# Kernel tuning notes

Measured on AMD Instinct MI355X. Metric: run time of the kernel, lower is better.

## Reference

```python
import jax, jax.numpy as jnp
import numpy as np

N_NODES = 100000
N_EDGES = 1600000
N_GRAPHS = 128
ATOM_F = 92
BOND_F = 41
EMB = 64
HID = 128
CHG = 16
N_LAYERS = 3
EPS = 1e-5


def setup_inputs() -> dict:
    key = jax.random.key(0)
    ks = jax.random.split(key, 32)
    s = 0.05
    inp = {
        "x": jax.random.normal(ks[0], (N_NODES, ATOM_F), jnp.float32),
        "edge_attr": jax.random.uniform(ks[1], (N_EDGES, BOND_F), jnp.float32),
        "charge": jax.random.normal(ks[2], (N_GRAPHS,), jnp.float32),
        "edge_index": jax.random.randint(ks[3], (2, N_EDGES), 0, N_NODES),
        "batch": jnp.sort(jax.random.randint(ks[4], (N_NODES,), 0, N_GRAPHS)),
        # embeddings
        "W_charge": jax.random.normal(ks[5], (1, CHG), jnp.float32) * s,
        "b_charge": jnp.zeros((CHG,), jnp.float32),
        "W_atom": jax.random.normal(ks[6], (ATOM_F + CHG, EMB), jnp.float32) * s,
        "b_atom": jnp.zeros((EMB,), jnp.float32),
        "W_bond": jax.random.normal(ks[7], (BOND_F, EMB), jnp.float32) * s,
        "b_bond": jnp.zeros((EMB,), jnp.float32),
        # conv layers (stacked over layer dim)
        "conv_eW1": jax.random.normal(ks[8], (N_LAYERS, 3 * EMB, EMB), jnp.float32) * s,
        "conv_eb1": jnp.zeros((N_LAYERS, EMB), jnp.float32),
        "conv_eW2": jax.random.normal(ks[9], (N_LAYERS, EMB, EMB), jnp.float32) * s,
        "conv_eb2": jnp.zeros((N_LAYERS, EMB), jnp.float32),
        "conv_nW1": jax.random.normal(ks[10], (N_LAYERS, 2 * EMB, EMB), jnp.float32) * s,
        "conv_nb1": jnp.zeros((N_LAYERS, EMB), jnp.float32),
        "conv_nW2": jax.random.normal(ks[11], (N_LAYERS, EMB, EMB), jnp.float32) * s,
        "conv_nb2": jnp.zeros((N_LAYERS, EMB), jnp.float32),
        "bn_gamma": jnp.ones((N_LAYERS, EMB), jnp.float32),
        "bn_beta": jnp.zeros((N_LAYERS, EMB), jnp.float32),
        # predictor
        "pW1": jax.random.normal(ks[12], (EMB, HID), jnp.float32) * s,
        "pb1": jnp.zeros((HID,), jnp.float32),
        "pW2": jax.random.normal(ks[13], (HID, HID), jnp.float32) * s,
        "pb2": jnp.zeros((HID,), jnp.float32),
        "pW3": jax.random.normal(ks[14], (HID, 1), jnp.float32) * s,
        "pb3": jnp.zeros((1,), jnp.float32),
    }
    return inp


def reference(x, edge_attr, charge, W_charge, b_charge, W_atom, b_atom,
              W_bond, b_bond, conv_eW1, conv_eb1, conv_eW2, conv_eb2,
              conv_nW1, conv_nb1, conv_nW2, conv_nb2, bn_gamma, bn_beta,
              pW1, pb1, pW2, pb2, pW3, pb3, edge_index, batch):
    sp = jax.nn.softplus
    n_nodes = x.shape[0]
    n_graphs = charge.shape[0]

    # early charge integration: per-graph charge embedding broadcast to nodes
    charge_feat = charge[:, None] @ W_charge + b_charge          # [B, CHG]
    x = jnp.concatenate([x, charge_feat[batch]], axis=1)          # [N, ATOM_F+CHG]
    x = x @ W_atom + b_atom                                       # [N, EMB]
    ea = edge_attr @ W_bond + b_bond                              # [E, EMB]

    row, col = edge_index[0], edge_index[1]
    for i in range(conv_eW1.shape[0]):
        xr, xc = x[row], x[col]                                   # gathers [E, EMB]
        # edge update: MLP on [x_row, x_col, edge_attr]
        e_in = jnp.concatenate([xr, xc, ea], axis=1)              # [E, 3*EMB]
        ea = sp(e_in @ conv_eW1[i] + conv_eb1[i]) @ conv_eW2[i] + conv_eb2[i]
        # node messages: MLP on [x_row, new edge_attr]
        m_in = jnp.concatenate([xr, ea], axis=1)                  # [E, 2*EMB]
        msg = sp(m_in @ conv_nW1[i] + conv_nb1[i]) @ conv_nW2[i] + conv_nb2[i]
        x_new = jax.ops.segment_sum(msg, col, num_segments=n_nodes)
        # BatchNorm1d (training-mode batch stats, biased variance)
        mean = jnp.mean(x_new, axis=0)
        var = jnp.var(x_new, axis=0)
        x_new = (x_new - mean) * jax.lax.rsqrt(var + EPS) * bn_gamma[i] + bn_beta[i]
        x = sp(x_new) + x                                         # residual

    # global mean pool over graphs
    sums = jax.ops.segment_sum(x, batch, num_segments=n_graphs)   # [B, EMB]
    cnt = jax.ops.segment_sum(jnp.ones((n_nodes, 1), x.dtype), batch, num_segments=n_graphs)
    g = sums / jnp.maximum(cnt, 1.0)

    # predictor MLP (dropout is identity in eval mode)
    h = sp(g @ pW1 + pb1)
    h = sp(h @ pW2 + pb2)
    out = h @ pW3 + pb3                                           # [B, 1]
    return out.squeeze(-1)
```

## Files before the change

### kernel.cpp

```cpp
#include <hip/hip_runtime.h>
#include <math.h>

typedef short v8s __attribute__((ext_vector_type(8)));
typedef float v4f __attribute__((ext_vector_type(4)));

__device__ __forceinline__ float sp_f(float x) {
  return fmaxf(x, 0.0f) + 0.69314718056f * __log2f(1.0f + __expf(-fabsf(x)));
}

__device__ __forceinline__ unsigned short f2bf(float f) {
  union { float f; unsigned u; } x; x.f = f;
  unsigned r = (x.u + 0x7FFF + ((x.u >> 16) & 1)) >> 16;
  return (unsigned short)r;
}

__device__ __forceinline__ float bf2f(unsigned short h) {
  union { unsigned u; float f; } x; x.u = ((unsigned)h) << 16;
  return x.f;
}

__global__ __launch_bounds__(256) void k_prep_wfrag(
    const float* __restrict__ eW1, const float* __restrict__ eW2,
    const float* __restrict__ nW1, const float* __restrict__ nW2,
    unsigned short* __restrict__ wfrag) {
  int i = blockIdx.x >> 2;
  int m = blockIdx.x & 3;
  const float* W;
  if (m == 0)      W = eW1 + (size_t)i * 192 * 64 + 128 * 64;
  else if (m == 1) W = eW2 + (size_t)i * 64 * 64;
  else if (m == 2) W = nW1 + (size_t)i * 128 * 64 + 64 * 64;
  else             W = nW2 + (size_t)i * 64 * 64;
  unsigned short* out = wfrag + ((size_t)i * 4 + m) * 4096;
  for (int f = threadIdx.x; f < 4096; f += 256) {
    int j = f & 7, ln = (f >> 3) & 63, kh = (f >> 9) & 1, ct = f >> 10;
    int k = kh * 32 + (ln >> 4) * 8 + j;
    int n = ct * 16 + (ln & 15);
    out[f] = f2bf(W[k * 64 + n]);
  }
}

__global__ __launch_bounds__(256) void k_embed_nodes(
    const float* __restrict__ x, const int* __restrict__ batch,
    const float* __restrict__ charge, const float* __restrict__ W_charge,
    const float* __restrict__ b_charge, const float* __restrict__ W_atom,
    const float* __restrict__ b_atom, float* __restrict__ xemb, int N) {
  __shared__ float sW[108 * 64];
  __shared__ float sX[128 * 92];
  __shared__ float sb[64];
  __shared__ float sWc[16];
  __shared__ float sbc[16];
  for (int i = threadIdx.x; i < 108 * 64; i += blockDim.x) sW[i] = W_atom[i];
  if (threadIdx.x < 64) sb[threadIdx.x] = b_atom[threadIdx.x];
  if (threadIdx.x < 16) {
    sWc[threadIdx.x] = W_charge[threadIdx.x];
    sbc[threadIdx.x] = b_charge[threadIdx.x];
  }
  int ntiles = (N + 127) >> 7;
  for (int tile = blockIdx.x; tile < ntiles; tile += gridDim.x) {
    int base = tile << 7;
    int cnt = N - base; if (cnt > 128) cnt = 128;
    __syncthreads();
    if (cnt == 128) {
      const float4* src = (const float4*)(x + (size_t)base * 92);
      for (int i = threadIdx.x; i < 2944; i += 256) ((float4*)sX)[i] = src[i];
    } else {
      for (int i = threadIdx.x; i < cnt * 92; i += 256)
        sX[i] = x[(size_t)base * 92 + i];
    }
    __syncthreads();
    int t = threadIdx.x;
    int node = t & 127, half = t >> 7;
    if (node < cnt) {
      int n = base + node;
      float acc[32];
#pragma unroll
      for (int j = 0; j < 32; ++j) acc[j] = sb[half * 32 + j];
      const float* xr = sX + node * 92;
      for (int k = 0; k < 92; ++k) {
        float a = xr[k];
        const float* wk = sW + k * 64 + half * 32;
#pragma unroll
        for (int j = 0; j < 32; ++j) acc[j] = fmaf(a, wk[j], acc[j]);
      }
      float ch = charge[batch[n]];
#pragma unroll
      for (int c = 0; c < 16; ++c) {
        float cf = fmaf(ch, sWc[c], sbc[c]);
        const float* wk = sW + (92 + c) * 64 + half * 32;
#pragma unroll
        for (int j = 0; j < 32; ++j) acc[j] = fmaf(cf, wk[j], acc[j]);
      }
      float* o = xemb + (size_t)n * 64 + half * 32;
#pragma unroll
      for (int q8 = 0; q8 < 8; ++q8)
        ((float4*)o)[q8] = make_float4(acc[4*q8], acc[4*q8+1], acc[4*q8+2], acc[4*q8+3]);
    }
  }
}

__global__ __launch_bounds__(256) void k_hist(const int* __restrict__ col,
                                              int* __restrict__ counts, int E) {
  int stride = gridDim.x * blockDim.x;
  for (int e = blockIdx.x * blockDim.x + threadIdx.x; e < E; e += stride)
    atomicAdd(&counts[col[e]], 1);
}

__global__ __launch_bounds__(256) void k_scan1(const int* __restrict__ counts,
                                               int* __restrict__ scan_tmp,
                                               int* __restrict__ bsum, int N) {
  __shared__ int sd[2][256];
  int t = threadIdx.x;
  int i = blockIdx.x * 256 + t;
  int v = (i < N) ? counts[i] : 0;
  sd[0][t] = v;
  __syncthreads();
  int s = 0;
#pragma unroll
  for (int off = 1; off < 256; off <<= 1) {
    int nv = sd[s][t];
    if (t >= off) nv += sd[s][t - off];
    sd[s ^ 1][t] = nv;
    s ^= 1;
    __syncthreads();
  }
  if (i < N) scan_tmp[i] = sd[s][t];
  if (t == 255) bsum[blockIdx.x] = sd[s][255];
}

__global__ __launch_bounds__(256) void k_scan2(int* __restrict__ b, int NB) {
  __shared__ int sd[2][256];
  __shared__ int carry_s;
  int t = threadIdx.x;
  if (t == 0) carry_s = 0;
  __syncthreads();
  for (int base = 0; base < NB; base += 256) {
    int i = base + t;
    int v = (i < NB) ? b[i] : 0;
    sd[0][t] = v;
    __syncthreads();
    int s = 0;
#pragma unroll
    for (int off = 1; off < 256; off <<= 1) {
      int nv = sd[s][t];
      if (t >= off) nv += sd[s][t - off];
      sd[s ^ 1][t] = nv;
      s ^= 1;
      __syncthreads();
    }
    int c = carry_s;
    int tot = sd[s][255];
    if (i < NB) b[i] = sd[s][t] + c;
    __syncthreads();
    if (t == 0) carry_s = c + tot;
    __syncthreads();
  }
}

__global__ __launch_bounds__(256) void k_scan3(const int* __restrict__ counts,
                                               const int* __restrict__ scan_tmp,
                                               const int* __restrict__ bsum,
                                               int* __restrict__ cursor, int N) {
  int i = blockIdx.x * 256 + threadIdx.x;
  if (i < N) {
    int base = (blockIdx.x > 0) ? bsum[blockIdx.x - 1] : 0;
    cursor[i] = scan_tmp[i] - counts[i] + base;
  }
}

__global__ __launch_bounds__(256) void k_scatter(
    const int* __restrict__ row, const int* __restrict__ col,
    int* __restrict__ cursor, int* __restrict__ pos,
    int* __restrict__ row_s, int* __restrict__ col_s, int E) {
  int stride = gridDim.x * blockDim.x;
  for (int e = blockIdx.x * blockDim.x + threadIdx.x; e < E; e += stride) {
    int c = col[e];
    int p = atomicAdd(&cursor[c], 1);
    pos[e] = p;
    row_s[p] = row[e];
    col_s[p] = c;
  }
}

__global__ __launch_bounds__(256) void k_embed_bonds_pos(
    const float* __restrict__ eattr, const int* __restrict__ pos,
    const float* __restrict__ W_bond, const float* __restrict__ b_bond,
    unsigned short* __restrict__ ea16, int E) {
  __shared__ float sW[41 * 64];
  __shared__ float sE[256 * 41];
  __shared__ float sb[64];
  for (int i = threadIdx.x; i < 41 * 64; i += blockDim.x) sW[i] = W_bond[i];
  if (threadIdx.x < 64) sb[threadIdx.x] = b_bond[threadIdx.x];
  int ntiles = (E + 255) >> 8;
  for (int tile = blockIdx.x; tile < ntiles; tile += gridDim.x) {
    int base = tile << 8;
    int cnt = E - base; if (cnt > 256) cnt = 256;
    __syncthreads();
    if (cnt == 256) {
      const float4* src = (const float4*)(eattr + (size_t)base * 41);
      for (int i = threadIdx.x; i < 2624; i += 256) ((float4*)sE)[i] = src[i];
    } else {
      for (int i = threadIdx.x; i < cnt * 41; i += 256)
        sE[i] = eattr[(size_t)base * 41 + i];
    }
    __syncthreads();
    int t = threadIdx.x;
    if (t < cnt) {
      float acc[64];
#pragma unroll
      for (int j = 0; j < 64; ++j) acc[j] = sb[j];
      const float* er = sE + t * 41;
      for (int k = 0; k < 41; ++k) {
        float a = er[k];
        const float* wk = sW + k * 64;
#pragma unroll
        for (int j = 0; j < 64; ++j) acc[j] = fmaf(a, wk[j], acc[j]);
      }
      size_t ob = (size_t)pos[base + t] * 64;
#pragma unroll
      for (int q8 = 0; q8 < 8; ++q8) {
        unsigned short tmp[8];
#pragma unroll
        for (int j = 0; j < 8; ++j) tmp[j] = f2bf(acc[q8 * 8 + j]);
        *(uint4*)&ea16[ob + q8 * 8] = *(uint4*)tmp;
      }
    }
  }
}

__device__ __forceinline__ void node_pre_body(
    const float* __restrict__ xr, const float* sWa, const float* sWb,
    const float* sWp, unsigned short* __restrict__ up16,
    unsigned short* __restrict__ v16, int n) {
  const float4* xr4 = (const float4*)xr;
  float u[64], p[64];
#pragma unroll
  for (int j = 0; j < 64; ++j) { u[j] = 0.f; p[j] = 0.f; }
  for (int k4 = 0; k4 < 16; ++k4) {
    float4 av = xr4[k4];
    const float* wa = sWa + k4 * 256;
    const float* wp = sWp + k4 * 256;
#pragma unroll
    for (int j = 0; j < 64; ++j) u[j] = fmaf(av.x, wa[j], u[j]);
#pragma unroll
    for (int j = 0; j < 64; ++j) p[j] = fmaf(av.x, wp[j], p[j]);
#pragma unroll
    for (int j = 0; j < 64; ++j) u[j] = fmaf(av.y, wa[64 + j], u[j]);
#pragma unroll
    for (int j = 0; j < 64; ++j) p[j] = fmaf(av.y, wp[64 + j], p[j]);
#pragma unroll
    for (int j = 0; j < 64; ++j) u[j] = fmaf(av.z, wa[128 + j], u[j]);
#pragma unroll
    for (int j = 0; j < 64; ++j) p[j] = fmaf(av.z, wp[128 + j], p[j]);
#pragma unroll
    for (int j = 0; j < 64; ++j) u[j] = fmaf(av.w, wa[192 + j], u[j]);
#pragma unroll
    for (int j = 0; j < 64; ++j) p[j] = fmaf(av.w, wp[192 + j], p[j]);
  }
  unsigned short* o = up16 + (size_t)n * 128;
#pragma unroll
  for (int q8 = 0; q8 < 8; ++q8) {
    unsigned short tmp[8];
#pragma unroll
    for (int j = 0; j < 8; ++j) {
      int i = q8 * 8 + j;
      tmp[j] = f2bf(u[((i & 3) << 4) | (i >> 2)]);
    }
    *(uint4*)&o[q8 * 8] = *(uint4*)tmp;
  }
#pragma unroll
  for (int q8 = 0; q8 < 8; ++q8) {
    unsigned short tmp[8];
#pragma unroll
    for (int j = 0; j < 8; ++j) {
      int i = q8 * 8 + j;
      tmp[j] = f2bf(p[((i & 3) << 4) | (i >> 2)]);
    }
    *(uint4*)&o[64 + q8 * 8] = *(uint4*)tmp;
  }
  float vv[64];
#pragma unroll
  for (int j = 0; j < 64; ++j) vv[j] = 0.f;
  for (int k4 = 0; k4 < 16; ++k4) {
    float4 av = xr4[k4];
    const float* wb = sWb + k4 * 256;
#pragma unroll
    for (int j = 0; j < 64; ++j) vv[j] = fmaf(av.x, wb[j], vv[j]);
#pragma unroll
    for (int j = 0; j < 64; ++j) vv[j] = fmaf(av.y, wb[64 + j], vv[j]);
#pragma unroll
    for (int j = 0; j < 64; ++j) vv[j] = fmaf(av.z, wb[128 + j], vv[j]);
#pragma unroll
    for (int j = 0; j < 64; ++j) vv[j] = fmaf(av.w, wb[192 + j], vv[j]);
  }
  unsigned short* ov = v16 + (size_t)n * 64;
#pragma unroll
  for (int q8 = 0; q8 < 8; ++q8) {
    unsigned short tmp[8];
#pragma unroll
    for (int j = 0; j < 8; ++j) {
      int i = q8 * 8 + j;
      tmp[j] = f2bf(vv[((i & 3) << 4) | (i >> 2)]);
    }
    *(uint4*)&ov[q8 * 8] = *(uint4*)tmp;
  }
}

__global__ __launch_bounds__(256) void k_node_pre(
    const float* __restrict__ xemb, const float* __restrict__ eW1,
    const float* __restrict__ nW1, unsigned short* __restrict__ up16,
    unsigned short* __restrict__ v16, int N) {
  __shared__ float sWa[64 * 64];
  __shared__ float sWb[64 * 64];
  __shared__ float sWp[64 * 64];
  for (int i = threadIdx.x; i < 64 * 64; i += blockDim.x) {
    sWa[i] = eW1[i];
    sWb[i] = eW1[64 * 64 + i];
    sWp[i] = nW1[i];
  }
  __syncthreads();
  int stride = gridDim.x * blockDim.x;
  for (int n = blockIdx.x * blockDim.x + threadIdx.x; n < N; n += stride)
    node_pre_body(xemb + (size_t)n * 64, sWa, sWb, sWp, up16, v16, n);
}

__global__ __launch_bounds__(256) void k_bn_pre(
    float* __restrict__ xemb, const float* __restrict__ xnew,
    const float* __restrict__ bnacc, const float* __restrict__ gamma,
    const float* __restrict__ beta, const float* __restrict__ eW1n,
    const float* __restrict__ nW1n, unsigned short* __restrict__ up16,
    unsigned short* __restrict__ v16, int N) {
  __shared__ float sWa[64 * 64];
  __shared__ float sWb[64 * 64];
  __shared__ float sWp[64 * 64];
  __shared__ float sscale[64], sshift[64];
  for (int i = threadIdx.x; i < 64 * 64; i += blockDim.x) {
    sWa[i] = eW1n[i];
    sWb[i] = eW1n[64 * 64 + i];
    sWp[i] = nW1n[i];
  }
  if (threadIdx.x < 64) {
    float inv = 1.0f / (float)N;
    float m = bnacc[threadIdx.x] * inv;
    float var = bnacc[64 + threadIdx.x] * inv - m * m;
    float rs = rsqrtf(var + 1e-5f);
    float g = gamma[threadIdx.x];
    sscale[threadIdx.x] = rs * g;
    sshift[threadIdx.x] = beta[threadIdx.x] - m * rs * g;
  }
  __syncthreads();
  int stride = gridDim.x * blockDim.x;
  for (int n = blockIdx.x * blockDim.x + threadIdx.x; n < N; n += stride) {
    float* xr = xemb + (size_t)n * 64;
#pragma unroll
    for (int q = 0; q < 16; ++q) {
      float4 xn4 = ((const float4*)(xnew + (size_t)n * 64))[q];
      float4 xo4 = ((const float4*)xr)[q];
      xo4.x += sp_f(fmaf(xn4.x, sscale[4*q+0], sshift[4*q+0]));
      xo4.y += sp_f(fmaf(xn4.y, sscale[4*q+1], sshift[4*q+1]));
      xo4.z += sp_f(fmaf(xn4.z, sscale[4*q+2], sshift[4*q+2]));
      xo4.w += sp_f(fmaf(xn4.w, sscale[4*q+3], sshift[4*q+3]));
      ((float4*)xr)[q] = xo4;
    }
    node_pre_body(xr, sWa, sWb, sWp, up16, v16, n);
  }
}

#define READ_FRAGS(P)                                                        \
  {                                                                          \
    const v8s* wp_ = (const v8s*)gWf + (P) * 512;                            \
    _Pragma("unroll") for (int ct = 0; ct < 4; ++ct)                         \
        _Pragma("unroll") for (int kh = 0; kh < 2; ++kh)                     \
            bfr[ct][kh] = wp_[(ct * 2 + kh) * 64 + l];                       \
    _Pragma("unroll") for (int rb = 0; rb < 2; ++rb)                         \
        _Pragma("unroll") for (int kh = 0; kh < 2; ++kh) {                   \
      int row_ = rbase + rb * 16 + c16;                                      \
      af[rb][kh] = *(const v8s*)&sA[row_ * 64 +                              \
                                    ((kh * 32 + q * 8) ^ ((row_ & 7) << 3))];\
    }                                                                        \
  }

#define DO_MFMA()                                                            \
  _Pragma("unroll") for (int rb = 0; rb < 2; ++rb)                           \
      _Pragma("unroll") for (int ct = 0; ct < 4; ++ct) {                     \
    v4f a_ = {0.f, 0.f, 0.f, 0.f};                                           \
    a_ = __builtin_amdgcn_mfma_f32_16x16x32_bf16(af[rb][0], bfr[ct][0], a_,  \
                                                 0, 0, 0);                   \
    a_ = __builtin_amdgcn_mfma_f32_16x16x32_bf16(af[rb][1], bfr[ct][1], a_,  \
                                                 0, 0, 0);                   \
    acc[rb][ct] = a_;                                                        \
  }

__global__ __launch_bounds__(256, 4) void k_edge_mfma(
    const int* __restrict__ row_s, const int* __restrict__ col_s,
    unsigned short* __restrict__ ea16, const unsigned short* __restrict__ up16,
    const unsigned short* __restrict__ v16,
    const unsigned short* __restrict__ gWf, const float* __restrict__ eb1,
    const float* __restrict__ eb2, const float* __restrict__ nb1,
    const float* __restrict__ nb2, float* __restrict__ xnew, int E) {
  __shared__ __align__(16) unsigned char smem[34304];
  unsigned short* sA = (unsigned short*)smem;
  float* msgb        = (float*)smem;
  float* sBb         = (float*)(smem + 32768);
  int* scol          = (int*)(smem + 33792);

  int tid = threadIdx.x;
  int te = blockIdx.x * 128;
  int w = tid >> 6, l = tid & 63, q = l >> 4, c16 = l & 15;
  int rbase = w * 32;

  int rid[2][4], cid[2][4], eid[2][4];
#pragma unroll
  for (int rb = 0; rb < 2; ++rb)
#pragma unroll
    for (int r = 0; r < 4; ++r) {
      int rit = rbase + rb * 16 + q * 4 + r;
      int e = te + rit;
      eid[rb][r] = e;
      int ec = e < E ? e : E - 1;
      rid[rb][r] = row_s[ec];
      cid[rb][r] = col_s[ec];
    }
  ushort4 uu_pf[2][4], vv_pf[2][4];
#pragma unroll
  for (int rb = 0; rb < 2; ++rb)
#pragma unroll
    for (int r = 0; r < 4; ++r) {
      uu_pf[rb][r] = *(const ushort4*)&up16[(size_t)rid[rb][r] * 128 + c16 * 4];
      vv_pf[rb][r] = *(const ushort4*)&v16[(size_t)cid[rb][r] * 64 + c16 * 4];
    }

  if (tid < 64) {
    sBb[0 * 64 + tid] = eb1[tid];
    sBb[1 * 64 + tid] = eb2[tid];
    sBb[2 * 64 + tid] = nb1[tid];
    sBb[3 * 64 + tid] = nb2[tid];
  }
  if (tid < 128) {
    int e = te + tid;
    scol[tid] = col_s[e < E ? e : E - 1];
  }
  for (int i = tid; i < 1024; i += 256) {
    int r = i >> 3, cc = i & 7;
    int e = te + r;
    if (e >= E) e = E - 1;
    uint4 d = *(const uint4*)&ea16[(size_t)e * 64 + cc * 8];
    *(uint4*)&sA[r * 64 + ((cc * 8) ^ ((r & 7) << 3))] = d;
  }

  v8s af[2][2];
  v8s bfr[4][2];
  v4f acc[2][4];

  __syncthreads();

  READ_FRAGS(0);
  DO_MFMA();
  ushort4 pp_pf[2][4];
#pragma unroll
  for (int rb = 0; rb < 2; ++rb)
#pragma unroll
    for (int r = 0; r < 4; ++r)
      pp_pf[rb][r] =
          *(const ushort4*)&up16[(size_t)rid[rb][r] * 128 + 64 + c16 * 4];
#pragma unroll
  for (int rb = 0; rb < 2; ++rb)
#pragma unroll
    for (int r = 0; r < 4; ++r) {
      int row = rbase + rb * 16 + q * 4 + r;
      const unsigned short* up_ = (const unsigned short*)&uu_pf[rb][r];
      const unsigned short* vp_ = (const unsigned short*)&vv_pf[rb][r];
#pragma unroll
      for (int ct = 0; ct < 4; ++ct) {
        int n = ct * 16 + c16;
        float t = acc[rb][ct][r] + sBb[n] + bf2f(up_[ct]) + bf2f(vp_[ct]);
        t = sp_f(t);
        sA[row * 64 + (n ^ ((row & 7) << 3))] = f2bf(t);
      }
    }

  READ_FRAGS(1);
  DO_MFMA();
#pragma unroll
  for (int rb = 0; rb < 2; ++rb)
#pragma unroll
    for (int ct = 0; ct < 4; ++ct) {
      int n = ct * 16 + c16;
#pragma unroll
      for (int r = 0; r < 4; ++r) {
        float en = acc[rb][ct][r] + sBb[64 + n];
        int row = rbase + rb * 16 + q * 4 + r;
        sA[row * 64 + (n ^ ((row & 7) << 3))] = f2bf(en);
      }
    }
  __syncthreads();
  for (int i = tid; i < 1024; i += 256) {
    int r = i >> 3, cc = i & 7;
    if (te + r < E) {
      uint4 d = *(const uint4*)&sA[r * 64 + ((cc * 8) ^ ((r & 7) << 3))];
      *(uint4*)&ea16[(size_t)(te + r) * 64 + cc * 8] = d;
    }
  }
  __syncthreads();

  READ_FRAGS(2);
  DO_MFMA();
#pragma unroll
  for (int rb = 0; rb < 2; ++rb)
#pragma unroll
    for (int r = 0; r < 4; ++r) {
      int row = rbase + rb * 16 + q * 4 + r;
      const unsigned short* pp_ = (const unsigned short*)&pp_pf[rb][r];
#pragma unroll
      for (int ct = 0; ct < 4; ++ct) {
        int n = ct * 16 + c16;
        float t2 = acc[rb][ct][r] + sBb[128 + n] + bf2f(pp_[ct]);
        t2 = sp_f(t2);
        sA[row * 64 + (n ^ ((row & 7) << 3))] = f2bf(t2);
      }
    }

  READ_FRAGS(3);
  __syncthreads();
  DO_MFMA();
#pragma unroll
  for (int rb = 0; rb < 2; ++rb)
#pragma unroll
    for (int ct = 0; ct < 4; ++ct) {
      int n = ct * 16 + c16;
#pragma unroll
      for (int r = 0; r < 4; ++r) {
        float msg = acc[rb][ct][r] + sBb[192 + n];
        int row = rbase + rb * 16 + q * 4 + r;
        msgb[row * 64 + n] = (eid[rb][r] < E) ? msg : 0.0f;
      }
    }
  __syncthreads();

  int nrows = E - te;
  if (nrows > 128) nrows = 128;
  for (int r0 = w; r0 < nrows; r0 += 4) {
    int c0 = scol[r0];
    if (r0 > 0 && scol[r0 - 1] == c0) continue;
    float s = 0.0f;
    int r = r0;
    do {
      s += msgb[r * 64 + l];
      ++r;
    } while (r < nrows && scol[r] == c0);
    atomicAdd(&xnew[(size_t)c0 * 64 + l], s);
  }
}

__global__ __launch_bounds__(256) void k_bn_stats(
    const float* __restrict__ xnew, float* __restrict__ bnacc, int N) {
  int t = threadIdx.x;
  int ch = t & 63;
  int sl = t >> 6;
  float s = 0.f, s2 = 0.f;
  for (int n = blockIdx.x * 4 + sl; n < N; n += gridDim.x * 4) {
    float v = xnew[(size_t)n * 64 + ch];
    s += v;
    s2 = fmaf(v, v, s2);
  }
  __shared__ float red[256], red2[256];
  red[t] = s;
  red2[t] = s2;
  __syncthreads();
  if (sl == 0) {
    s = red[ch] + red[64 + ch] + red[128 + ch] + red[192 + ch];
    s2 = red2[ch] + red2[64 + ch] + red2[128 + ch] + red2[192 + ch];
    atomicAdd(&bnacc[ch], s);
    atomicAdd(&bnacc[64 + ch], s2);
  }
}

__global__ __launch_bounds__(256) void k_bn_apply(
    float* __restrict__ x, const float* __restrict__ xnew,
    const float* __restrict__ bnacc, const float* __restrict__ gamma,
    const float* __restrict__ beta, int N) {
  __shared__ float sscale[64], sshift[64];
  if (threadIdx.x < 64) {
    float inv = 1.0f / (float)N;
    float m = bnacc[threadIdx.x] * inv;
    float var = bnacc[64 + threadIdx.x] * inv - m * m;
    float rs = rsqrtf(var + 1e-5f);
    float g = gamma[threadIdx.x];
    sscale[threadIdx.x] = rs * g;
    sshift[threadIdx.x] = beta[threadIdx.x] - m * rs * g;
  }
  __syncthreads();
  size_t total = (size_t)N * 64;
  size_t stride = (size_t)gridDim.x * blockDim.x;
  for (size_t i = (size_t)blockIdx.x * blockDim.x + threadIdx.x; i < total; i += stride) {
    int ch = (int)(i & 63);
    float v = fmaf(xnew[i], sscale[ch], sshift[ch]);
    x[i] += sp_f(v);
  }
}

__device__ __forceinline__ int lbound(const int* a, int n, int key) {
  int lo = 0, hi = n;
  while (lo < hi) {
    int mid = (lo + hi) >> 1;
    if (a[mid] < key) lo = mid + 1; else hi = mid;
  }
  return lo;
}

__global__ __launch_bounds__(256) void k_pool_pred(
    const float* __restrict__ x, const int* __restrict__ batch, int N,
    const float* __restrict__ pW1, const float* __restrict__ pb1,
    const float* __restrict__ pW2, const float* __restrict__ pb2,
    const float* __restrict__ pW3, const float* __restrict__ pb3,
    float* __restrict__ out) {
  int b = blockIdx.x;
  int lo = lbound(batch, N, b);
  int hi = lbound(batch, N, b + 1);
  int t = threadIdx.x;
  int ch = t & 63;
  int sl = t >> 6;
  float s = 0.f;
  for (int n = lo + sl; n < hi; n += 4) s += x[(size_t)n * 64 + ch];
  __shared__ float red4[4][64];
  __shared__ float sg[64];
  __shared__ float sh1[128];
  __shared__ float red[128];
  red4[sl][ch] = s;
  __syncthreads();
  if (t < 64) {
    float tot = red4[0][t] + red4[1][t] + red4[2][t] + red4[3][t];
    float cnt = (float)(hi - lo);
    sg[t] = tot / fmaxf(cnt, 1.0f);
  }
  __syncthreads();
  if (t < 128) {
    float h = pb1[t];
    for (int k = 0; k < 64; ++k) h = fmaf(sg[k], pW1[k * 128 + t], h);
    sh1[t] = sp_f(h);
  }
  __syncthreads();
  if (t < 128) {
    float h = pb2[t];
    for (int k = 0; k < 128; ++k) h = fmaf(sh1[k], pW2[k * 128 + t], h);
    red[t] = sp_f(h) * pW3[t];
  }
  __syncthreads();
  for (int off = 64; off > 0; off >>= 1) {
    if (t < off) red[t] += red[t + off];
    __syncthreads();
  }
  if (t == 0) out[b] = red[0] + pb3[0];
}

extern "C" void kernel_launch(void* const* d_in, const int* in_sizes, int n_in,
                              void* d_out, int out_size, void* d_ws, size_t ws_size,
                              hipStream_t stream) {
  const float* x         = (const float*)d_in[0];
  const float* edge_attr = (const float*)d_in[1];
  const float* charge    = (const float*)d_in[2];
  const int*   eidx      = (const int*)d_in[3];
  const int*   batch     = (const int*)d_in[4];
  const float* W_charge  = (const float*)d_in[5];
  const float* b_charge  = (const float*)d_in[6];
  const float* W_atom    = (const float*)d_in[7];
  const float* b_atom    = (const float*)d_in[8];
  const float* W_bond    = (const float*)d_in[9];
  const float* b_bond    = (const float*)d_in[10];
  const float* eW1 = (const float*)d_in[11];
  const float* eb1 = (const float*)d_in[12];
  const float* eW2 = (const float*)d_in[13];
  const float* eb2 = (const float*)d_in[14];
  const float* nW1 = (const float*)d_in[15];
  const float* nb1 = (const float*)d_in[16];
  const float* nW2 = (const float*)d_in[17];
  const float* nb2 = (const float*)d_in[18];
  const float* gam = (const float*)d_in[19];
  const float* bet = (const float*)d_in[20];
  const float* pW1 = (const float*)d_in[21];
  const float* pb1 = (const float*)d_in[22];
  const float* pW2 = (const float*)d_in[23];
  const float* pb2 = (const float*)d_in[24];
  const float* pW3 = (const float*)d_in[25];
  const float* pb3 = (const float*)d_in[26];

  int N = in_sizes[4];
  int E = in_sizes[3] / 2;
  int B = in_sizes[2];
  const int* row = eidx;
  const int* col = eidx + E;

  char* wptr = (char*)d_ws;
  unsigned short* ea16 = (unsigned short*)wptr; wptr += (((size_t)E * 64 * 2 + 255) & ~255ull);
  unsigned short* up16 = (unsigned short*)wptr; wptr += (((size_t)N * 128 * 2 + 255) & ~255ull);
  unsigned short* v16  = (unsigned short*)wptr; wptr += (((size_t)N * 64 * 2 + 255) & ~255ull);
  unsigned short* wfrag = (unsigned short*)wptr; wptr += 12 * 4096 * 2;
  float* xemb = (float*)wptr; wptr += (size_t)N * 64 * 4;
  float* xnew = (float*)wptr; wptr += (size_t)N * 64 * 4;
  float* bnacc = (float*)wptr; wptr += 256 * 4;
  int* counts = (int*)wptr;   wptr += (size_t)N * 4;
  int* scan_tmp = (int*)wptr; wptr += (size_t)N * 4;
  int* cursor = (int*)wptr;   wptr += (size_t)N * 4;
  int* bsum = (int*)wptr;     wptr += 4096;
  int* pos = (int*)wptr;      wptr += (size_t)E * 4;
  int* row_s = (int*)wptr;    wptr += (size_t)E * 4;
  int* col_s = (int*)wptr;    wptr += (size_t)E * 4;

  int NB = (N + 255) / 256;

  k_prep_wfrag<<<12, 256, 0, stream>>>(eW1, eW2, nW1, nW2, wfrag);
  hipMemsetAsync(counts, 0, (size_t)N * 4, stream);
  k_hist<<<2048, 256, 0, stream>>>(col, counts, E);
  k_scan1<<<NB, 256, 0, stream>>>(counts, scan_tmp, bsum, N);
  k_scan2<<<1, 256, 0, stream>>>(bsum, NB);
  k_scan3<<<NB, 256, 0, stream>>>(counts, scan_tmp, bsum, cursor, N);
  k_scatter<<<2048, 256, 0, stream>>>(row, col, cursor, pos, row_s, col_s, E);

  int ntilesN = (N + 127) / 128;
  k_embed_nodes<<<ntilesN, 256, 0, stream>>>(x, batch, charge, W_charge,
                                             b_charge, W_atom, b_atom, xemb, N);
  k_embed_bonds_pos<<<2048, 256, 0, stream>>>(edge_attr, pos, W_bond, b_bond,
                                              ea16, E);
  k_node_pre<<<NB, 256, 0, stream>>>(xemb, eW1, nW1, up16, v16, N);

  int gridE = (E + 127) / 128;
  for (int i = 0; i < 3; ++i) {
    hipMemsetAsync(xnew, 0, (size_t)N * 64 * 4, stream);
    hipMemsetAsync(bnacc, 0, 256 * 4, stream);
    k_edge_mfma<<<gridE, 256, 0, stream>>>(
        row_s, col_s, ea16, up16, v16, wfrag + (size_t)i * 16384,
        eb1 + (size_t)i * 64, eb2 + (size_t)i * 64, nb1 + (size_t)i * 64,
        nb2 + (size_t)i * 64, xnew, E);
    k_bn_stats<<<1024, 256, 0, stream>>>(xnew, bnacc, N);
    if (i < 2) {
      k_bn_pre<<<NB, 256, 0, stream>>>(
          xemb, xnew, bnacc, gam + (size_t)i * 64, bet + (size_t)i * 64,
          eW1 + (size_t)(i + 1) * 192 * 64, nW1 + (size_t)(i + 1) * 128 * 64,
          up16, v16, N);
    } else {
      k_bn_apply<<<4096, 256, 0, stream>>>(xemb, xnew, bnacc,
                                           gam + (size_t)i * 64,
                                           bet + (size_t)i * 64, N);
    }
  }

  k_pool_pred<<<B, 256, 0, stream>>>(xemb, batch, N, pW1, pb1, pW2, pb2,
                                     pW3, pb3, (float*)d_out);
}
```

Measured before the change: 2.198 ms.

## Use MFMA for bond embedding, interleave up16 layout, skip final ea store, reduce atomics

```diff
diff --git a/kernel.cpp b/kernel.cpp
--- a/kernel.cpp
+++ b/kernel.cpp
@@ -22,7 +22,17 @@
 __global__ __launch_bounds__(256) void k_prep_wfrag(
     const float* __restrict__ eW1, const float* __restrict__ eW2,
     const float* __restrict__ nW1, const float* __restrict__ nW2,
-    unsigned short* __restrict__ wfrag) {
+    const float* __restrict__ W_bond, unsigned short* __restrict__ wfrag) {
+  if (blockIdx.x == 12) {
+    unsigned short* out = wfrag + 12 * 4096;
+    for (int f = threadIdx.x; f < 4096; f += 256) {
+      int j = f & 7, ln = (f >> 3) & 63, kh = (f >> 9) & 1, ct = f >> 10;
+      int k = kh * 32 + (ln >> 4) * 8 + j;
+      int n = ct * 16 + (ln & 15);
+      out[f] = (k < 41) ? f2bf(W_bond[k * 64 + n]) : 0;
+    }
+    return;
+  }
   int i = blockIdx.x >> 2;
   int m = blockIdx.x & 3;
   const float* W;
@@ -181,47 +191,77 @@
   }
 }
 
-__global__ __launch_bounds__(256) void k_embed_bonds_pos(
+__global__ __launch_bounds__(256) void k_embed_bonds_mfma(
     const float* __restrict__ eattr, const int* __restrict__ pos,
-    const float* __restrict__ W_bond, const float* __restrict__ b_bond,
+    const unsigned short* __restrict__ gWb, const float* __restrict__ b_bond,
     unsigned short* __restrict__ ea16, int E) {
-  __shared__ float sW[41 * 64];
-  __shared__ float sE[256 * 41];
+  __shared__ unsigned short sA[128 * 64];
   __shared__ float sb[64];
-  for (int i = threadIdx.x; i < 41 * 64; i += blockDim.x) sW[i] = W_bond[i];
-  if (threadIdx.x < 64) sb[threadIdx.x] = b_bond[threadIdx.x];
-  int ntiles = (E + 255) >> 8;
+  __shared__ int spos[128];
+  int tid = threadIdx.x;
+  int w = tid >> 6, l = tid & 63, q = l >> 4, c16 = l & 15;
+  int rbase = w * 32;
+  if (tid < 64) sb[tid] = b_bond[tid];
+  int ntiles = (E + 127) >> 7;
   for (int tile = blockIdx.x; tile < ntiles; tile += gridDim.x) {
-    int base = tile << 8;
-    int cnt = E - base; if (cnt > 256) cnt = 256;
-    __syncthreads();
-    if (cnt == 256) {
-      const float4* src = (const float4*)(eattr + (size_t)base * 41);
-      for (int i = threadIdx.x; i < 2624; i += 256) ((float4*)sE)[i] = src[i];
-    } else {
-      for (int i = threadIdx.x; i < cnt * 41; i += 256)
-        sE[i] = eattr[(size_t)base * 41 + i];
-    }
-    __syncthreads();
-    int t = threadIdx.x;
-    if (t < cnt) {
-      float acc[64];
-#pragma unroll
-      for (int j = 0; j < 64; ++j) acc[j] = sb[j];
-      const float* er = sE + t * 41;
-      for (int k = 0; k < 41; ++k) {
-        float a = er[k];
-        const float* wk = sW + k * 64;
-#pragma unroll
-        for (int j = 0; j < 64; ++j) acc[j] = fmaf(a, wk[j], acc[j]);
-      }
-      size_t ob = (size_t)pos[base + t] * 64;
-#pragma unroll
-      for (int q8 = 0; q8 < 8; ++q8) {
-        unsigned short tmp[8];
-#pragma unroll
-        for (int j = 0; j < 8; ++j) tmp[j] = f2bf(acc[q8 * 8 + j]);
-        *(uint4*)&ea16[ob + q8 * 8] = *(uint4*)tmp;
+    int te = tile << 7;
+    int cnt = E - te; if (cnt > 128) cnt = 128;
+    __syncthreads();
+    uint4 z = make_uint4(0, 0, 0, 0);
+    for (int i = tid; i < 1024; i += 256) ((uint4*)sA)[i] = z;
+    __syncthreads();
+    int nflt = cnt * 41;
+    for (int i = tid; i < nflt; i += 256) {
+      int r = i / 41, k = i - r * 41;
+      float v = eattr[(size_t)te * 41 + i];
+      sA[r * 64 + (k ^ ((r & 7) << 3))] = f2bf(v);
+    }
+    if (tid < 128) spos[tid] = (te + tid < E) ? pos[te + tid] : -1;
+    __syncthreads();
+    v8s bfr[4][2], af[2][2];
+    v4f acc[2][4];
+    const v8s* wp_ = (const v8s*)gWb;
+#pragma unroll
+    for (int ct = 0; ct < 4; ++ct)
+#pragma unroll
+      for (int kh = 0; kh < 2; ++kh)
+        bfr[ct][kh] = wp_[(ct * 2 + kh) * 64 + l];
+#pragma unroll
+    for (int rb = 0; rb < 2; ++rb)
+#pragma unroll
+      for (int kh = 0; kh < 2; ++kh) {
+        int row_ = rbase + rb * 16 + c16;
+        af[rb][kh] = *(const v8s*)&sA[row_ * 64 +
+                                      ((kh * 32 + q * 8) ^ ((row_ & 7) << 3))];
+      }
+#pragma unroll
+    for (int rb = 0; rb < 2; ++rb)
+#pragma unroll
+      for (int ct = 0; ct < 4; ++ct) {
+        v4f a_ = {0.f, 0.f, 0.f, 0.f};
+        a_ = __builtin_amdgcn_mfma_f32_16x16x32_bf16(af[rb][0], bfr[ct][0], a_, 0, 0, 0);
+        a_ = __builtin_amdgcn_mfma_f32_16x16x32_bf16(af[rb][1], bfr[ct][1], a_, 0, 0, 0);
+        acc[rb][ct] = a_;
+      }
+#pragma unroll
+    for (int rb = 0; rb < 2; ++rb)
+#pragma unroll
+      for (int ct = 0; ct < 4; ++ct) {
+        int n = ct * 16 + c16;
+#pragma unroll
+        for (int r = 0; r < 4; ++r) {
+          float v = acc[rb][ct][r] + sb[n];
+          int row = rbase + rb * 16 + q * 4 + r;
+          sA[row * 64 + (n ^ ((row & 7) << 3))] = f2bf(v);
+        }
+      }
+    __syncthreads();
+    for (int i = tid; i < 1024; i += 256) {
+      int r = i >> 3, cc = i & 7;
+      int p = spos[r];
+      if (p >= 0) {
+        uint4 d = *(const uint4*)&sA[r * 64 + ((cc * 8) ^ ((r & 7) << 3))];
+        *(uint4*)&ea16[(size_t)p * 64 + cc * 8] = d;
       }
     }
   }
@@ -258,24 +298,12 @@
   }
   unsigned short* o = up16 + (size_t)n * 128;
 #pragma unroll
-  for (int q8 = 0; q8 < 8; ++q8) {
+  for (int q8 = 0; q8 < 16; ++q8) {
     unsigned short tmp[8];
 #pragma unroll
-    for (int j = 0; j < 8; ++j) {
-      int i = q8 * 8 + j;
-      tmp[j] = f2bf(u[((i & 3) << 4) | (i >> 2)]);
-    }
+    for (int j = 0; j < 8; ++j)
+      tmp[j] = f2bf(j < 4 ? u[j * 16 + q8] : p[(j - 4) * 16 + q8]);
     *(uint4*)&o[q8 * 8] = *(uint4*)tmp;
-  }
-#pragma unroll
-  for (int q8 = 0; q8 < 8; ++q8) {
-    unsigned short tmp[8];
-#pragma unroll
-    for (int j = 0; j < 8; ++j) {
-      int i = q8 * 8 + j;
-      tmp[j] = f2bf(p[((i & 3) << 4) | (i >> 2)]);
-    }
-    *(uint4*)&o[64 + q8 * 8] = *(uint4*)tmp;
   }
   float vv[64];
 #pragma unroll
@@ -396,7 +424,8 @@
     const unsigned short* __restrict__ v16,
     const unsigned short* __restrict__ gWf, const float* __restrict__ eb1,
     const float* __restrict__ eb2, const float* __restrict__ nb1,
-    const float* __restrict__ nb2, float* __restrict__ xnew, int E) {
+    const float* __restrict__ nb2, float* __restrict__ xnew, int E,
+    int store_ea) {
   __shared__ __align__(16) unsigned char smem[34304];
   unsigned short* sA = (unsigned short*)smem;
   float* msgb        = (float*)smem;
@@ -413,19 +442,19 @@
   for (int rb = 0; rb < 2; ++rb)
 #pragma unroll
     for (int r = 0; r < 4; ++r) {
-      int rit = rbase + rb * 16 + q * 4 + r;
-      int e = te + rit;
+      int e = te + rbase + rb * 16 + q * 4 + r;
       eid[rb][r] = e;
       int ec = e < E ? e : E - 1;
       rid[rb][r] = row_s[ec];
       cid[rb][r] = col_s[ec];
     }
-  ushort4 uu_pf[2][4], vv_pf[2][4];
+  uint4 upv_pf[2][4];
+  ushort4 vv_pf[2][4];
 #pragma unroll
   for (int rb = 0; rb < 2; ++rb)
 #pragma unroll
     for (int r = 0; r < 4; ++r) {
-      uu_pf[rb][r] = *(const ushort4*)&up16[(size_t)rid[rb][r] * 128 + c16 * 4];
+      upv_pf[rb][r] = *(const uint4*)&up16[(size_t)rid[rb][r] * 128 + c16 * 8];
       vv_pf[rb][r] = *(const ushort4*)&v16[(size_t)cid[rb][r] * 64 + c16 * 4];
     }
 
@@ -455,24 +484,17 @@
 
   READ_FRAGS(0);
   DO_MFMA();
-  ushort4 pp_pf[2][4];
 #pragma unroll
   for (int rb = 0; rb < 2; ++rb)
 #pragma unroll
-    for (int r = 0; r < 4; ++r)
-      pp_pf[rb][r] =
-          *(const ushort4*)&up16[(size_t)rid[rb][r] * 128 + 64 + c16 * 4];
-#pragma unroll
-  for (int rb = 0; rb < 2; ++rb)
-#pragma unroll
     for (int r = 0; r < 4; ++r) {
+      const unsigned short* uv = (const unsigned short*)&upv_pf[rb][r];
+      const unsigned short* vp_ = (const unsigned short*)&vv_pf[rb][r];
       int row = rbase + rb * 16 + q * 4 + r;
-      const unsigned short* up_ = (const unsigned short*)&uu_pf[rb][r];
-      const unsigned short* vp_ = (const unsigned short*)&vv_pf[rb][r];
 #pragma unroll
       for (int ct = 0; ct < 4; ++ct) {
         int n = ct * 16 + c16;
-        float t = acc[rb][ct][r] + sBb[n] + bf2f(up_[ct]) + bf2f(vp_[ct]);
+        float t = acc[rb][ct][r] + sBb[n] + bf2f(uv[ct]) + bf2f(vp_[ct]);
         t = sp_f(t);
         sA[row * 64 + (n ^ ((row & 7) << 3))] = f2bf(t);
       }
@@ -493,11 +515,13 @@
       }
     }
   __syncthreads();
-  for (int i = tid; i < 1024; i += 256) {
-    int r = i >> 3, cc = i & 7;
-    if (te + r < E) {
-      uint4 d = *(const uint4*)&sA[r * 64 + ((cc * 8) ^ ((r & 7) << 3))];
-      *(uint4*)&ea16[(size_t)(te + r) * 64 + cc * 8] = d;
+  if (store_ea) {
+    for (int i = tid; i < 1024; i += 256) {
+      int r = i >> 3, cc = i & 7;
+      if (te + r < E) {
+        uint4 d = *(const uint4*)&sA[r * 64 + ((cc * 8) ^ ((r & 7) << 3))];
+        *(uint4*)&ea16[(size_t)(te + r) * 64 + cc * 8] = d;
+      }
     }
   }
   __syncthreads();
@@ -508,12 +532,12 @@
   for (int rb = 0; rb < 2; ++rb)
 #pragma unroll
     for (int r = 0; r < 4; ++r) {
+      const unsigned short* uv = (const unsigned short*)&upv_pf[rb][r];
       int row = rbase + rb * 16 + q * 4 + r;
-      const unsigned short* pp_ = (const unsigned short*)&pp_pf[rb][r];
 #pragma unroll
       for (int ct = 0; ct < 4; ++ct) {
         int n = ct * 16 + c16;
-        float t2 = acc[rb][ct][r] + sBb[128 + n] + bf2f(pp_[ct]);
+        float t2 = acc[rb][ct][r] + sBb[128 + n] + bf2f(uv[4 + ct]);
         t2 = sp_f(t2);
         sA[row * 64 + (n ^ ((row & 7) << 3))] = f2bf(t2);
       }
@@ -547,7 +571,10 @@
       s += msgb[r * 64 + l];
       ++r;
     } while (r < nrows && scol[r] == c0);
-    atomicAdd(&xnew[(size_t)c0 * 64 + l], s);
+    if (r0 > 0 && r < nrows)
+      xnew[(size_t)c0 * 64 + l] = s;
+    else
+      atomicAdd(&xnew[(size_t)c0 * 64 + l], s);
   }
 }
 
@@ -693,7 +720,7 @@
   unsigned short* ea16 = (unsigned short*)wptr; wptr += (((size_t)E * 64 * 2 + 255) & ~255ull);
   unsigned short* up16 = (unsigned short*)wptr; wptr += (((size_t)N * 128 * 2 + 255) & ~255ull);
   unsigned short* v16  = (unsigned short*)wptr; wptr += (((size_t)N * 64 * 2 + 255) & ~255ull);
-  unsigned short* wfrag = (unsigned short*)wptr; wptr += 12 * 4096 * 2;
+  unsigned short* wfrag = (unsigned short*)wptr; wptr += 13 * 4096 * 2;
   float* xemb = (float*)wptr; wptr += (size_t)N * 64 * 4;
   float* xnew = (float*)wptr; wptr += (size_t)N * 64 * 4;
   float* bnacc = (float*)wptr; wptr += 256 * 4;
@@ -707,7 +734,7 @@
 
   int NB = (N + 255) / 256;
 
-  k_prep_wfrag<<<12, 256, 0, stream>>>(eW1, eW2, nW1, nW2, wfrag);
+  k_prep_wfrag<<<13, 256, 0, stream>>>(eW1, eW2, nW1, nW2, W_bond, wfrag);
   hipMemsetAsync(counts, 0, (size_t)N * 4, stream);
   k_hist<<<2048, 256, 0, stream>>>(col, counts, E);
   k_scan1<<<NB, 256, 0, stream>>>(counts, scan_tmp, bsum, N);
@@ -718,8 +745,9 @@
   int ntilesN = (N + 127) / 128;
   k_embed_nodes<<<ntilesN, 256, 0, stream>>>(x, batch, charge, W_charge,
                                              b_charge, W_atom, b_atom, xemb, N);
-  k_embed_bonds_pos<<<2048, 256, 0, stream>>>(edge_attr, pos, W_bond, b_bond,
-                                              ea16, E);
+  k_embed_bonds_mfma<<<2048, 256, 0, stream>>>(edge_attr, pos,
+                                               wfrag + 12 * 4096, b_bond,
+                                               ea16, E);
   k_node_pre<<<NB, 256, 0, stream>>>(xemb, eW1, nW1, up16, v16, N);
 
   int gridE = (E + 127) / 128;
@@ -729,7 +757,7 @@
     k_edge_mfma<<<gridE, 256, 0, stream>>>(
         row_s, col_s, ea16, up16, v16, wfrag + (size_t)i * 16384,
         eb1 + (size_t)i * 64, eb2 + (size_t)i * 64, nb1 + (size_t)i * 64,
-        nb2 + (size_t)i * 64, xnew, E);
+        nb2 + (size_t)i * 64, xnew, E, (i < 2) ? 1 : 0);
     k_bn_stats<<<1024, 256, 0, stream>>>(xnew, bnacc, N);
     if (i < 2) {
       k_bn_pre<<<NB, 256, 0, stream>>>(
```

Result: no change. 2.174 ms (-1.1%).
